# Optimization experiments

Hardware: AMD Instinct MI355X
Metric: run time of the kernel (lower is better)

Reference implementation:

```python
import jax, jax.numpy as jnp
import numpy as np

N_NODES, N_EDGES, N_CRYS = 50000, 1200000, 256
AF, NF, NR = 64, 64, 16
INV_SQRT_2 = 1.0 / 2.0 ** 0.5
EPS = 1e-5


def crystal_norm(x, idx, nseg, gamma, beta):
    # per-crystal, per-feature mean/var normalization
    cnt = jnp.maximum(jax.ops.segment_sum(jnp.ones((x.shape[0],), x.dtype), idx, nseg), 1.0)[:, None]
    mean = jax.ops.segment_sum(x, idx, nseg) / cnt
    d = x - mean[idx]
    var = jax.ops.segment_sum(d * d, idx, nseg) / cnt
    return d / jnp.sqrt(var[idx] + EPS) * gamma + beta


def setup_inputs() -> dict:
    key = jax.random.key(0)
    ks = jax.random.split(key, 16)
    s = 0.05
    return {
        'atom_fea': jax.random.normal(ks[0], (N_NODES, AF), jnp.float32),
        'edge': jax.random.normal(ks[1], (N_EDGES, NF), jnp.float32),
        'rbf': jax.random.uniform(ks[2], (N_EDGES, NR), jnp.float32),
        'nbr_fea_idx': jax.random.randint(ks[3], (N_EDGES, 2), 0, N_NODES),
        'crystal_atom_idx': jax.random.randint(ks[4], (N_NODES,), 0, N_CRYS),
        'crystal_edge_idx': jax.random.randint(ks[5], (N_EDGES,), 0, N_CRYS),
        'W_rbf': jax.random.normal(ks[6], (NR, NF), jnp.float32) * s,
        'W_full': jax.random.normal(ks[7], (2 * AF + NF, 2 * AF), jnp.float32) * s,
        'W_mask': jax.random.normal(ks[8], (AF, 1), jnp.float32) * s,
        'g1': jnp.ones((2 * AF,), jnp.float32),
        'b1': jnp.zeros((2 * AF,), jnp.float32),
        'g2': jnp.ones((AF,), jnp.float32),
        'b2': jnp.zeros((AF,), jnp.float32),
        'Wr1a': jax.random.normal(ks[9], (AF, AF // 2), jnp.float32) * s,
        'Wr1b': jax.random.normal(ks[10], (AF // 2, AF), jnp.float32) * s,
        'Wr2a': jax.random.normal(ks[11], (AF, AF // 2), jnp.float32) * s,
        'Wr2b': jax.random.normal(ks[12], (AF // 2, AF), jnp.float32) * s,
    }


def reference(atom_fea, edge, rbf, nbr_fea_idx, crystal_atom_idx, crystal_edge_idx,
              W_rbf, W_full, W_mask, g1, b1, g2, b2, Wr1a, Wr1b, Wr2a, Wr2b):
    rbf_h = rbf @ W_rbf                                   # [E, NF]
    sum_idx = nbr_fea_idx[:, 0]
    nbr_fea = edge * rbf_h                                # [E, NF]
    atom_nbr_fea = atom_fea[nbr_fea_idx].reshape(-1, 2 * AF)  # [E, 2*AF]
    total = jnp.concatenate([atom_nbr_fea, nbr_fea], axis=1)  # [E, 2*AF+NF]
    gated = total @ W_full                                # [E, 2*AF]
    gated = crystal_norm(gated, crystal_edge_idx, N_CRYS, g1, b1)
    nbr_filter, nbr_core = gated[:, :AF], gated[:, AF:]
    nbr_filter = jax.nn.sigmoid(nbr_filter @ W_mask)      # [E, 1]
    nbr_core = jax.nn.relu(nbr_core)
    msg = nbr_filter * nbr_core                           # [E, AF]
    cnt = jnp.maximum(jax.ops.segment_sum(jnp.ones((msg.shape[0],), msg.dtype), sum_idx, N_NODES), 1.0)[:, None]
    nbr_sumed = jax.ops.segment_sum(msg, sum_idx, N_NODES) / cnt  # scatter-mean
    nbr_sumed = crystal_norm(nbr_sumed, crystal_atom_idx, N_CRYS, g2, b2)
    # 2 residual blocks: out = (x + relu(relu(x W_a) W_b)) / sqrt(2)
    h = jax.nn.relu(jax.nn.relu(nbr_sumed @ Wr1a) @ Wr1b)
    nbr_sumed = (nbr_sumed + h) * INV_SQRT_2
    h = jax.nn.relu(jax.nn.relu(nbr_sumed @ Wr2a) @ Wr2b)
    nbr_sumed = (nbr_sumed + h) * INV_SQRT_2
    return INV_SQRT_2 * jax.nn.relu(atom_fea + nbr_sumed)
```

## Files before the change

### kernel.cpp

```cpp
#include <hip/hip_runtime.h>
#include <hip/hip_bf16.h>

typedef __attribute__((ext_vector_type(8))) short bfrag;
typedef __attribute__((ext_vector_type(4))) float f4;

__device__ __forceinline__ unsigned short f2bf(float f){
  unsigned b = __float_as_uint(f);
  b = (b + 0x7fffu + ((b >> 16) & 1u)) >> 16;
  return (unsigned short)b;
}
__device__ __forceinline__ unsigned pk2bf(float a, float b){
  return (unsigned)f2bf(a) | ((unsigned)f2bf(b) << 16);
}
__device__ __forceinline__ float bf2f(unsigned short u){
  return __uint_as_float(((unsigned)u) << 16);
}
__device__ __forceinline__ bfrag pack8(float4 x, float4 y){
  bfrag r;
  r[0]=(short)f2bf(x.x); r[1]=(short)f2bf(x.y); r[2]=(short)f2bf(x.z); r[3]=(short)f2bf(x.w);
  r[4]=(short)f2bf(y.x); r[5]=(short)f2bf(y.y); r[6]=(short)f2bf(y.z); r[7]=(short)f2bf(y.w);
  return r;
}

__global__ __launch_bounds__(256) void k_acvt(const float* __restrict__ atom,
                                              unsigned short* __restrict__ atomBF, int total8){
  int i = blockIdx.x*256 + threadIdx.x;
  if (i >= total8) return;
  const float4* src = (const float4*)atom + (size_t)i*2;
  float4 x = src[0], y = src[1];
  *(bfrag*)(atomBF + (size_t)i*8) = pack8(x, y);
}

__global__ __launch_bounds__(64) void k_prep(const float* __restrict__ Wf, unsigned short* __restrict__ Bpack){
  int l = threadIdx.x; int f = blockIdx.x; int ks = f >> 3; int nt = f & 7;
  int kg = l >> 4; int nn = l & 15;
#pragma unroll
  for (int j = 0; j < 8; ++j){
    int k;
    if (ks < 4) k = ks*32 + kg*8 + j;
    else        k = 128 + (ks-4)*32 + ((j>>2)<<4) + kg*4 + (j&3);
    Bpack[((size_t)f*64 + l)*8 + j] = f2bf(Wf[(size_t)k*128 + nt*16 + nn]);
  }
}

__global__ __launch_bounds__(256) void k_pre(const int* __restrict__ cidxe, int E,
                                             const int* __restrict__ cidxn, int NN,
                                             const int* __restrict__ nbr,
                                             int* __restrict__ ccnte, int* __restrict__ ccntn,
                                             int* __restrict__ ncnt){
  __shared__ int he[256], hn[256];
  int t = threadIdx.x;
  he[t] = 0; hn[t] = 0;
  __syncthreads();
  for (size_t i = (size_t)blockIdx.x*256 + t; i < (size_t)E; i += (size_t)gridDim.x*256){
    atomicAdd(&he[cidxe[i]], 1);
    atomicAdd(&ncnt[nbr[2*i]], 1);
  }
  for (size_t i = (size_t)blockIdx.x*256 + t; i < (size_t)NN; i += (size_t)gridDim.x*256)
    atomicAdd(&hn[cidxn[i]], 1);
  __syncthreads();
  if (he[t]) atomicAdd(&ccnte[t], he[t]);
  if (hn[t]) atomicAdd(&ccntn[t], hn[t]);
}

__global__ __launch_bounds__(1024) void k_scans(const int* __restrict__ ncnt, int NN,
                                                int* __restrict__ offs, int* __restrict__ cursor,
                                                const int* __restrict__ ccnte, const int* __restrict__ ccntn,
                                                int* __restrict__ ceoffs, int* __restrict__ cecur,
                                                int* __restrict__ cnoffs, int* __restrict__ cncur){
  int tid = threadIdx.x;
  if (blockIdx.x == 0){
    __shared__ int part[1024];
    int chunk = (NN + 1023) >> 10;
    int base = tid*chunk;
    int s = 0;
    for (int i = 0; i < chunk; ++i){ int p = base + i; if (p < NN) s += ncnt[p]; }
    part[tid] = s;
    __syncthreads();
    for (int d = 1; d < 1024; d <<= 1){
      int v = (tid >= d) ? part[tid - d] : 0;
      __syncthreads();
      part[tid] += v;
      __syncthreads();
    }
    int run = (tid == 0) ? 0 : part[tid-1];
    for (int i = 0; i < chunk; ++i){
      int p = base + i;
      if (p < NN){ offs[p] = run; cursor[p] = run; run += ncnt[p]; }
    }
    if (tid == 1023) offs[NN] = part[1023];
  } else {
    __shared__ int sh[256];
    const int* cnt = (blockIdx.x == 2) ? ccntn : ccnte;
    int* off = (blockIdx.x == 2) ? cnoffs : ceoffs;
    int* cur = (blockIdx.x == 2) ? cncur  : cecur;
    int v = 0;
    if (tid < 256){ v = cnt[tid]; sh[tid] = v; }
    __syncthreads();
    for (int d = 1; d < 256; d <<= 1){
      int x = (tid >= d && tid < 256) ? sh[tid - d] : 0;
      __syncthreads();
      if (tid < 256) sh[tid] += x;
      __syncthreads();
    }
    if (tid < 256){
      off[tid] = sh[tid] - v; cur[tid] = sh[tid] - v;
      if (tid == 255) off[256] = sh[255];
    }
  }
}

__global__ __launch_bounds__(256) void k_scatter2(const int* __restrict__ nbr, const int* __restrict__ cidxe,
                                                  int E, int* __restrict__ cursor, int4* __restrict__ edat,
                                                  int* __restrict__ gcur, int* __restrict__ celist){
  __shared__ int lhist[256], lbase[256], lcur[256];
  int t = threadIdx.x;
  lhist[t] = 0; lcur[t] = 0;
  __syncthreads();
  int base = blockIdx.x*1024;
  int end = min(base + 1024, E);
  for (int i = base + t; i < end; i += 256) atomicAdd(&lhist[cidxe[i]], 1);
  __syncthreads();
  if (lhist[t]) lbase[t] = atomicAdd(&gcur[t], lhist[t]);
  __syncthreads();
  for (int i = base + t; i < end; i += 256){
    int cr = cidxe[i];
    int n = nbr[2*(size_t)i];
    int j = nbr[2*(size_t)i + 1];
    int pos = atomicAdd(&cursor[n], 1);
    edat[pos] = make_int4(n, j, i, cr);
    int lp = atomicAdd(&lcur[cr], 1);
    celist[lbase[cr] + lp] = pos;
  }
}

__global__ __launch_bounds__(256) void k_cscatter(const int* __restrict__ idx, int n,
                                                  int* __restrict__ gcur, int* __restrict__ outl){
  __shared__ int lhist[256], lbase[256], lcur[256];
  int t = threadIdx.x;
  lhist[t] = 0; lcur[t] = 0;
  __syncthreads();
  int base = blockIdx.x*4096;
  int end = min(base + 4096, n);
  for (int i = base + t; i < end; i += 256) atomicAdd(&lhist[idx[i]], 1);
  __syncthreads();
  if (lhist[t]) lbase[t] = atomicAdd(&gcur[t], lhist[t]);
  __syncthreads();
  for (int i = base + t; i < end; i += 256){
    int b = idx[i];
    int p = atomicAdd(&lcur[b], 1);
    outl[lbase[b] + p] = i;
  }
}

struct TileRegs {
  bfrag a0, a1, a2, a3;
  bfrag rf;
  float4 re0, re1, re2, re3;
};

__device__ __forceinline__ TileRegs load_tile(const unsigned short* __restrict__ atomBF,
                                              const float* __restrict__ edgef,
                                              const float* __restrict__ rbff, const int4* __restrict__ edat,
                                              int r0, int e16, int g, int E){
  TileRegs R;
  int er = r0 + e16;
  if (er >= E) er = 0;
  const int4 ed = edat[er];
  const unsigned short* Ai = atomBF + (size_t)ed.x*64;
  const unsigned short* Aj = atomBF + (size_t)ed.y*64;
  R.a0 = *(const bfrag*)(Ai + g*8);
  R.a1 = *(const bfrag*)(Ai + 32 + g*8);
  R.a2 = *(const bfrag*)(Aj + g*8);
  R.a3 = *(const bfrag*)(Aj + 32 + g*8);
  float4 rr0 = make_float4(0.f,0.f,0.f,0.f);
  float4 rr1 = make_float4(0.f,0.f,0.f,0.f);
  if (g < 2){
    const float4* rp = (const float4*)(rbff + (size_t)ed.z*16 + g*8);
    rr0 = rp[0]; rr1 = rp[1];
  }
  const float4* ep = (const float4*)(edgef + (size_t)ed.z*64);
  R.re0 = ep[g]; R.re1 = ep[4+g]; R.re2 = ep[8+g]; R.re3 = ep[12+g];
  R.rf = pack8(rr0, rr1);
  return R;
}

template<int FNT0, int FNT1>
__global__ __launch_bounds__(512) void k_gemm(const unsigned short* __restrict__ atomBF,
                                              const float* __restrict__ edgef,
                                              const float* __restrict__ rbff, const int4* __restrict__ edat,
                                              const float* __restrict__ Wrbf,
                                              const unsigned short* __restrict__ Bpack,
                                              unsigned short* __restrict__ gated, int gstride, int colOff,
                                              int tBase, int tEnd, int E)
{
  __shared__ uint4 sBv[3072];
  const unsigned short* sB = (const unsigned short*)sBv;
  const int bid = (blockIdx.x & 7)*(gridDim.x >> 3) + (blockIdx.x >> 3);
  const int lane = threadIdx.x & 63;
  const int wid  = (bid*512 + threadIdx.x) >> 6;
  const int nW   = gridDim.x*8;
  const int e16  = lane & 15;
  const int g    = lane >> 4;
  const f4 zero = {0.f, 0.f, 0.f, 0.f};

  {
    const uint4* src = (const uint4*)Bpack;
    for (int i = threadIdx.x; i < 3072; i += 512) sBv[i] = src[i];
  }

  bfrag wf[4];
#pragma unroll
  for (int ct = 0; ct < 4; ++ct){
#pragma unroll
    for (int i = 0; i < 8; ++i){
      float v = (g < 2) ? Wrbf[(g*8 + i)*64 + ct*16 + e16] : 0.f;
      wf[ct][i] = (short)f2bf(v);
    }
  }
  __syncthreads();

  int t = tBase + wid;
  if (t >= tEnd) return;
  TileRegs cur = load_tile(atomBF, edgef, rbff, edat, t*16, e16, g, E);

  while (true){
    const int tn = t + nW;
    const bool more = tn < tEnd;
    TileRegs nxt;
    if (more) nxt = load_tile(atomBF, edgef, rbff, edat, tn*16, e16, g, E);
    __builtin_amdgcn_sched_barrier(0);

    int er = t*16 + e16;
    const bool rowOK = er < E;
    if (!rowOK) er = 0;

    f4 h0 = __builtin_amdgcn_mfma_f32_16x16x32_bf16(wf[0], cur.rf, zero, 0, 0, 0);
    f4 h1 = __builtin_amdgcn_mfma_f32_16x16x32_bf16(wf[1], cur.rf, zero, 0, 0, 0);
    f4 h2 = __builtin_amdgcn_mfma_f32_16x16x32_bf16(wf[2], cur.rf, zero, 0, 0, 0);
    f4 h3 = __builtin_amdgcn_mfma_f32_16x16x32_bf16(wf[3], cur.rf, zero, 0, 0, 0);

    bfrag aops[6];
    aops[0] = cur.a0; aops[1] = cur.a1; aops[2] = cur.a2; aops[3] = cur.a3;
    const float* pe0 = (const float*)&cur.re0;
    const float* pe1 = (const float*)&cur.re1;
    const float* pe2 = (const float*)&cur.re2;
    const float* pe3 = (const float*)&cur.re3;
#pragma unroll
    for (int r = 0; r < 4; ++r){
      aops[4][r]   = (short)f2bf(h0[r]*pe0[r]);
      aops[4][4+r] = (short)f2bf(h1[r]*pe1[r]);
      aops[5][r]   = (short)f2bf(h2[r]*pe2[r]);
      aops[5][4+r] = (short)f2bf(h3[r]*pe3[r]);
    }

    unsigned short* orow = gated + (size_t)er*(size_t)gstride - colOff;
#pragma unroll
    for (int f_nt = FNT0; f_nt < FNT1; ++f_nt){
      const unsigned short* bls = sB + ((size_t)(f_nt*64 + lane))*8;
      f4 acc = zero;
#pragma unroll
      for (int ks = 0; ks < 6; ++ks){
        bfrag b = *(const bfrag*)(bls + (size_t)ks*4096);
        acc = __builtin_amdgcn_mfma_f32_16x16x32_bf16(b, aops[ks], acc, 0, 0, 0);
      }
      if (rowOK){
        uint2 pk;
        pk.x = pk2bf(acc[0], acc[1]);
        pk.y = pk2bf(acc[2], acc[3]);
        *(uint2*)(orow + f_nt*16 + g*4) = pk;
      }
    }

    if (!more) break;
    cur = nxt;
    t = tn;
  }
}

__global__ __launch_bounds__(256) void k_cstats128(const unsigned short* __restrict__ gated,
                                                   const int* __restrict__ coffs, const int* __restrict__ celist,
                                                   float* __restrict__ pstat){
  int cr = blockIdx.x >> 3, s = blockIdx.x & 7;
  int t = threadIdx.x, w = t >> 6, lane = t & 63;
  int sub = lane >> 4, ch = lane & 15;
  int o0 = coffs[cr], o1 = coffs[cr+1];
  long long L = o1 - o0;
  int lo = o0 + (int)(L*s/8), hi = o0 + (int)(L*(s+1)/8);
  float S[8], Q[8];
#pragma unroll
  for (int j = 0; j < 8; ++j){ S[j] = 0.f; Q[j] = 0.f; }
  for (int p = lo + w*4; p < hi; p += 16){
    int q = p + sub;
    if (q < hi){
      int e = celist[q];
      uint4 vv = *(const uint4*)(gated + (size_t)e*128 + ch*8);
      unsigned uu0 = vv.x, uu1 = vv.y, uu2 = vv.z, uu3 = vv.w;
      float a0 = bf2f((unsigned short)(uu0 & 0xffffu)), b0 = bf2f((unsigned short)(uu0 >> 16));
      float a1 = bf2f((unsigned short)(uu1 & 0xffffu)), b1 = bf2f((unsigned short)(uu1 >> 16));
      float a2 = bf2f((unsigned short)(uu2 & 0xffffu)), b2 = bf2f((unsigned short)(uu2 >> 16));
      float a3 = bf2f((unsigned short)(uu3 & 0xffffu)), b3 = bf2f((unsigned short)(uu3 >> 16));
      S[0] += a0; Q[0] += a0*a0;  S[1] += b0; Q[1] += b0*b0;
      S[2] += a1; Q[2] += a1*a1;  S[3] += b1; Q[3] += b1*b1;
      S[4] += a2; Q[4] += a2*a2;  S[5] += b2; Q[5] += b2*b2;
      S[6] += a3; Q[6] += a3*a3;  S[7] += b3; Q[7] += b3*b3;
    }
  }
#pragma unroll
  for (int j = 0; j < 8; ++j){
    S[j] += __shfl_xor(S[j], 16, 64); S[j] += __shfl_xor(S[j], 32, 64);
    Q[j] += __shfl_xor(Q[j], 16, 64); Q[j] += __shfl_xor(Q[j], 32, 64);
  }
  __shared__ float sP[4][256];
  if (sub == 0){
#pragma unroll
    for (int j = 0; j < 8; ++j){
      sP[w][ch*16 + j]     = S[j];
      sP[w][ch*16 + 8 + j] = Q[j];
    }
  }
  __syncthreads();
  float v = sP[0][t] + sP[1][t] + sP[2][t] + sP[3][t];
  pstat[((size_t)blockIdx.x << 8) + t] = v;
}

__global__ __launch_bounds__(256) void k_cstats64(const unsigned short* __restrict__ gated,
                                                  const int* __restrict__ coffs, const int* __restrict__ celist,
                                                  float* __restrict__ pstat){
  int cr = blockIdx.x >> 3, s = blockIdx.x & 7;
  int t = threadIdx.x, w = t >> 6, lane = t & 63;
  int o0 = coffs[cr], o1 = coffs[cr+1];
  long long L = o1 - o0;
  int lo = o0 + (int)(L*s/8), hi = o0 + (int)(L*(s+1)/8);
  float S=0.f, Q=0.f;
  for (int p = lo + w*8; p < hi; p += 32){
#pragma unroll
    for (int u = 0; u < 8; ++u){
      if (p + u < hi){
        int e = celist[p+u];
        float a = bf2f(gated[(size_t)e*64 + lane]);
        S += a; Q += a*a;
      }
    }
  }
  __shared__ float sP[4][128];
  sP[w][lane*2+0]=S; sP[w][lane*2+1]=Q;
  __syncthreads();
  if (t < 128){
    float v = sP[0][t] + sP[1][t] + sP[2][t] + sP[3][t];
    pstat[((size_t)blockIdx.x << 7) + t] = v;
  }
}

__global__ __launch_bounds__(256) void k_cnstats(const float* __restrict__ nacc, const int* __restrict__ ncnt,
                                                 const int* __restrict__ coffs, const int* __restrict__ cnlist,
                                                 float* __restrict__ pstat){
  int cr = blockIdx.x >> 1, s = blockIdx.x & 1;
  int t = threadIdx.x, w = t >> 6, lane = t & 63;
  int sub = lane >> 4, c4 = lane & 15;
  int o0 = coffs[cr], o1 = coffs[cr+1];
  long long L = o1 - o0;
  int lo = o0 + (int)(L*s/2), hi = o0 + (int)(L*(s+1)/2);
  float S[4], Q[4];
#pragma unroll
  for (int j = 0; j < 4; ++j){ S[j] = 0.f; Q[j] = 0.f; }
  for (int p = lo + w*4; p < hi; p += 16){
    int q = p + sub;
    if (q < hi){
      int n = cnlist[q];
      float inv = 1.f / fmaxf((float)ncnt[n], 1.f);
      float4 v = *(const float4*)(nacc + (size_t)n*64 + c4*4);
      float a0 = v.x*inv, a1 = v.y*inv, a2 = v.z*inv, a3 = v.w*inv;
      S[0] += a0; Q[0] += a0*a0;
      S[1] += a1; Q[1] += a1*a1;
      S[2] += a2; Q[2] += a2*a2;
      S[3] += a3; Q[3] += a3*a3;
    }
  }
#pragma unroll
  for (int j = 0; j < 4; ++j){
    S[j] += __shfl_xor(S[j], 16, 64); S[j] += __shfl_xor(S[j], 32, 64);
    Q[j] += __shfl_xor(Q[j], 16, 64); Q[j] += __shfl_xor(Q[j], 32, 64);
  }
  __shared__ float sP[4][128];
  if (sub == 0){
#pragma unroll
    for (int j = 0; j < 4; ++j){
      sP[w][(c4*4 + j)*2]     = S[j];
      sP[w][(c4*4 + j)*2 + 1] = Q[j];
    }
  }
  __syncthreads();
  if (t < 128){
    float v = sP[0][t] + sP[1][t] + sP[2][t] + sP[3][t];
    pstat[((size_t)blockIdx.x << 7) + t] = v;
  }
}

__global__ __launch_bounds__(256) void k_red128f(const float* __restrict__ pstat, const int* __restrict__ ccnt,
                                                 const float* __restrict__ gamma, const float* __restrict__ beta,
                                                 const float* __restrict__ Wm,
                                                 float* __restrict__ sc, float* __restrict__ sh,
                                                 float* __restrict__ w2, float* __restrict__ fb){
  int idx = blockIdx.x*256 + threadIdx.x;
  int cr = idx >> 7, col = idx & 127;
  int vS = ((col >> 3) << 4) + (col & 7);
  float S=0.f, Q=0.f;
  for (int s2 = 0; s2 < 8; ++s2){
    const float* b = pstat + ((size_t)(cr*8 + s2) << 8);
    S += b[vS]; Q += b[vS + 8];
  }
  float cnt = fmaxf((float)ccnt[cr], 1.f);
  float mean = S/cnt;
  float var = fmaxf(Q/cnt - mean*mean, 0.f);
  float r = 1.f / sqrtf(var + 1e-5f);
  float g = r*gamma[col];
  float shv = beta[col] - mean*g;
  sc[cr*128 + col] = g;
  sh[cr*128 + col] = shv;

  __shared__ float red[256];
  float contrib = 0.f;
  if (col < 64){
    float wmv = Wm[col];
    w2[cr*64 + col] = g*wmv;
    contrib = shv*wmv;
  }
  red[threadIdx.x] = contrib;
  __syncthreads();
  int lc = threadIdx.x & 127;
  for (int d = 32; d > 0; d >>= 1){
    if (lc < d) red[threadIdx.x] += red[threadIdx.x + d];
    __syncthreads();
  }
  if (lc == 0) fb[cr] = red[threadIdx.x];
}

__global__ __launch_bounds__(256) void k_red64(const float* __restrict__ pstat, int nsplit,
                                               const int* __restrict__ ccnt,
                                               const float* __restrict__ gamma, const float* __restrict__ beta,
                                               float* __restrict__ sc, float* __restrict__ sh,
                                               int stride, int colOff){
  int idx = blockIdx.x*256 + threadIdx.x;
  int cr = idx >> 6, col = idx & 63;
  int vS = col*2;
  float S=0.f, Q=0.f;
  for (int s2 = 0; s2 < nsplit; ++s2){
    const float* b = pstat + ((size_t)(cr*nsplit + s2) << 7);
    S += b[vS]; Q += b[vS+1];
  }
  float cnt = fmaxf((float)ccnt[cr], 1.f);
  float mean = S/cnt;
  float var = fmaxf(Q/cnt - mean*mean, 0.f);
  float r = 1.f / sqrtf(var + 1e-5f);
  float g = r*gamma[col];
  sc[cr*stride + colOff + col] = g;
  sh[cr*stride + colOff + col] = beta[col] - mean*g;
}

__global__ __launch_bounds__(256) void k_fprep(const float* __restrict__ scE, const float* __restrict__ shE,
                                               const float* __restrict__ Wm, float* __restrict__ w2,
                                               float* __restrict__ fb){
  int t = threadIdx.x, w = t >> 6, lane = t & 63;
  int cr = blockIdx.x*4 + w;
  float wm = Wm[lane];
  w2[cr*64 + lane] = scE[cr*128 + lane]*wm;
  float b = shE[cr*128 + lane]*wm;
#pragma unroll
  for (int d = 1; d < 64; d <<= 1) b += __shfl_xor(b, d, 64);
  if (lane == 0) fb[cr] = b;
}

__global__ __launch_bounds__(256) void k_filter(const unsigned short* __restrict__ gated, int gst,
                                                const int4* __restrict__ edat, const float* __restrict__ w2,
                                                const float* __restrict__ fb, float* __restrict__ filt, int E){
  size_t r = (size_t)blockIdx.x*256 + threadIdx.x;
  if (r >= (size_t)E) return;
  int cr = edat[r].w;
  const uint4* row = (const uint4*)(gated + r*(size_t)gst);
  const float4* wr = (const float4*)(w2 + cr*64);
  float logit = fb[cr];
#pragma unroll
  for (int j = 0; j < 8; ++j){
    uint4 v = row[j];
    float4 wa = wr[2*j], wb = wr[2*j+1];
    logit += bf2f((unsigned short)(v.x & 0xffffu))*wa.x + bf2f((unsigned short)(v.x >> 16))*wa.y;
    logit += bf2f((unsigned short)(v.y & 0xffffu))*wa.z + bf2f((unsigned short)(v.y >> 16))*wa.w;
    logit += bf2f((unsigned short)(v.z & 0xffffu))*wb.x + bf2f((unsigned short)(v.z >> 16))*wb.y;
    logit += bf2f((unsigned short)(v.w & 0xffffu))*wb.z + bf2f((unsigned short)(v.w >> 16))*wb.w;
  }
  filt[r] = 1.f / (1.f + __expf(-logit));
}

__global__ __launch_bounds__(256) void k_msgf8(const unsigned short* __restrict__ gated,
                                               const int4* __restrict__ edat,
                                               const int* __restrict__ offs,
                                               const float* __restrict__ scE, const float* __restrict__ shE,
                                               const float* __restrict__ w2, const float* __restrict__ fb,
                                               float* __restrict__ nacc, int NN){
  int w = threadIdx.x >> 6, lane = threadIdx.x & 63;
  int n = blockIdx.x*4 + w;
  if (n >= NN) return;
  int sub = lane >> 3, c8 = lane & 7;
  float a0=0.f,a1=0.f,a2=0.f,a3=0.f,a4=0.f,a5=0.f,a6=0.f,a7=0.f;
  int p0 = offs[n], p1 = offs[n+1];

  int p = p0;
  bool any = p < p1;
  int4 ed; uint4 vf, vc;
  if (any){
    int q = p + sub; if (q >= p1) q = p;
    ed = edat[q];
    vf = *(const uint4*)(gated + (size_t)q*128 + c8*8);
    vc = *(const uint4*)(gated + (size_t)q*128 + 64 + c8*8);
  }
  while (any){
    const int pn = p + 8;
    const bool anyN = pn < p1;
    int4 edN; uint4 vfN, vcN;
    if (anyN){
      int qn = pn + sub; if (qn >= p1) qn = pn;
      edN = edat[qn];
      vfN = *(const uint4*)(gated + (size_t)qn*128 + c8*8);
      vcN = *(const uint4*)(gated + (size_t)qn*128 + 64 + c8*8);
    }
    __builtin_amdgcn_sched_barrier(0);

    const bool ok = (p + sub) < p1;
    int cr = ed.w;
    const float4* wvp = (const float4*)(w2 + cr*64 + c8*8);
    float4 wv0 = wvp[0], wv1 = wvp[1];
    float part = bf2f((unsigned short)(vf.x & 0xffffu))*wv0.x
               + bf2f((unsigned short)(vf.x >> 16))*wv0.y
               + bf2f((unsigned short)(vf.y & 0xffffu))*wv0.z
               + bf2f((unsigned short)(vf.y >> 16))*wv0.w
               + bf2f((unsigned short)(vf.z & 0xffffu))*wv1.x
               + bf2f((unsigned short)(vf.z >> 16))*wv1.y
               + bf2f((unsigned short)(vf.w & 0xffffu))*wv1.z
               + bf2f((unsigned short)(vf.w >> 16))*wv1.w;
#pragma unroll
    for (int d = 1; d < 8; d <<= 1) part += __shfl_xor(part, d, 64);
    float f = 1.f / (1.f + __expf(-(part + fb[cr])));
    const float4* scp = (const float4*)(scE + cr*128 + 64 + c8*8);
    const float4* shp = (const float4*)(shE + cr*128 + 64 + c8*8);
    float4 s0 = scp[0], s1 = scp[1];
    float4 h0 = shp[0], h1 = shp[1];
    if (ok){
      a0 += f*fmaxf(bf2f((unsigned short)(vc.x & 0xffffu))*s0.x + h0.x, 0.f);
      a1 += f*fmaxf(bf2f((unsigned short)(vc.x >> 16))*s0.y + h0.y, 0.f);
      a2 += f*fmaxf(bf2f((unsigned short)(vc.y & 0xffffu))*s0.z + h0.z, 0.f);
      a3 += f*fmaxf(bf2f((unsigned short)(vc.y >> 16))*s0.w + h0.w, 0.f);
      a4 += f*fmaxf(bf2f((unsigned short)(vc.z & 0xffffu))*s1.x + h1.x, 0.f);
      a5 += f*fmaxf(bf2f((unsigned short)(vc.z >> 16))*s1.y + h1.y, 0.f);
      a6 += f*fmaxf(bf2f((unsigned short)(vc.w & 0xffffu))*s1.z + h1.z, 0.f);
      a7 += f*fmaxf(bf2f((unsigned short)(vc.w >> 16))*s1.w + h1.w, 0.f);
    }
    if (!anyN) break;
    ed = edN; vf = vfN; vc = vcN; p = pn;
  }
#pragma unroll
  for (int d = 8; d < 64; d <<= 1){
    a0 += __shfl_xor(a0, d, 64); a1 += __shfl_xor(a1, d, 64);
    a2 += __shfl_xor(a2, d, 64); a3 += __shfl_xor(a3, d, 64);
    a4 += __shfl_xor(a4, d, 64); a5 += __shfl_xor(a5, d, 64);
    a6 += __shfl_xor(a6, d, 64); a7 += __shfl_xor(a7, d, 64);
  }
  if (lane < 8){
    float4 o0; o0.x = a0; o0.y = a1; o0.z = a2; o0.w = a3;
    float4 o1; o1.x = a4; o1.y = a5; o1.z = a6; o1.w = a7;
    float4* dst = (float4*)(nacc + (size_t)n*64 + (size_t)c8*8);
    dst[0] = o0; dst[1] = o1;
  }
}

__global__ __launch_bounds__(256) void k_msg3(const unsigned short* __restrict__ gated, int gst, int colBase,
                                              const int4* __restrict__ edat, const float* __restrict__ filt,
                                              const int* __restrict__ offs,
                                              const float* __restrict__ scE, const float* __restrict__ shE,
                                              int scOff, float* __restrict__ nacc, int NN){
  int w = threadIdx.x >> 6, lane = threadIdx.x & 63;
  int n = blockIdx.x*4 + w;
  if (n >= NN) return;
  int sub = lane >> 5, c2 = lane & 31;
  float a0 = 0.f, a1 = 0.f;
  int p0 = offs[n], p1 = offs[n+1];
  for (int p = p0; p < p1; p += 2){
    int idx = p + sub;
    bool ok = idx < p1;
    int q = ok ? idx : p;
    unsigned v = *(const unsigned*)(gated + (size_t)q*gst + colBase + c2*2);
    float f = filt[q];
    int cr = edat[q].w;
    float2 sc2 = *(const float2*)(scE + cr*128 + scOff + c2*2);
    float2 sh2 = *(const float2*)(shE + cr*128 + scOff + c2*2);
    if (ok){
      float g0 = bf2f((unsigned short)(v & 0xffffu));
      float g1 = bf2f((unsigned short)(v >> 16));
      a0 += f*fmaxf(g0*sc2.x + sh2.x, 0.f);
      a1 += f*fmaxf(g1*sc2.y + sh2.y, 0.f);
    }
  }
  a0 += __shfl_xor(a0, 32, 64);
  a1 += __shfl_xor(a1, 32, 64);
  if (lane < 32) *(float2*)(nacc + (size_t)n*64 + (size_t)c2*2) = make_float2(a0, a1);
}

__global__ __launch_bounds__(256) void k_final(const float* __restrict__ nacc, const int* __restrict__ ncnt,
                                               const int* __restrict__ cidx, const float* __restrict__ nsc,
                                               const float* __restrict__ nsh, const float* __restrict__ W1a,
                                               const float* __restrict__ W1b, const float* __restrict__ W2a,
                                               const float* __restrict__ W2b, const float* __restrict__ atom,
                                               float* __restrict__ out, int NN)
{
  __shared__ float sW[4][2048];
  __shared__ float hbuf[8192];
  int tid = threadIdx.x;
  for (int i = tid; i < 2048; i += 256){
    sW[0][i] = W1a[i]; sW[1][i] = W1b[i]; sW[2][i] = W2a[i]; sW[3][i] = W2b[i];
  }
  __syncthreads();
  int n = blockIdx.x*256 + tid;
  if (n >= NN) return;
  const float ISQ2 = 0.70710678118654752440f;
  int cr = cidx[n];
  float inv = 1.f / fmaxf((float)ncnt[n], 1.f);
  float x[64];
  const float4* src = (const float4*)(nacc + (size_t)n*64);
#pragma unroll
  for (int j = 0; j < 16; ++j){
    float4 v = src[j];
    x[4*j] = v.x*inv; x[4*j+1] = v.y*inv; x[4*j+2] = v.z*inv; x[4*j+3] = v.w*inv;
  }
#pragma unroll
  for (int c = 0; c < 64; ++c)
    x[c] = x[c]*nsc[cr*64 + c] + nsh[cr*64 + c];

  for (int blk = 0; blk < 2; ++blk){
    const float* sa = sW[blk*2];
    const float* sb = sW[blk*2 + 1];
    for (int j = 0; j < 32; ++j){
      float s = 0.f;
#pragma unroll
      for (int k = 0; k < 64; ++k) s += x[k]*sa[k*32 + j];
      hbuf[tid*32 + (j ^ (tid & 31))] = fmaxf(s, 0.f);
    }
    float x2[64];
#pragma unroll
    for (int c = 0; c < 64; ++c) x2[c] = 0.f;
    for (int j = 0; j < 32; ++j){
      float hj = hbuf[tid*32 + (j ^ (tid & 31))];
#pragma unroll
      for (int c = 0; c < 64; ++c) x2[c] += hj*sb[j*64 + c];
    }
#pragma unroll
    for (int c = 0; c < 64; ++c)
      x[c] = (x[c] + fmaxf(x2[c], 0.f))*ISQ2;
  }
  const float4* ap = (const float4*)(atom + (size_t)n*64);
  float4* op = (float4*)(out + (size_t)n*64);
#pragma unroll
  for (int j = 0; j < 16; ++j){
    float4 av = ap[j]; float4 o;
    o.x = ISQ2*fmaxf(av.x + x[4*j],   0.f);
    o.y = ISQ2*fmaxf(av.y + x[4*j+1], 0.f);
    o.z = ISQ2*fmaxf(av.z + x[4*j+2], 0.f);
    o.w = ISQ2*fmaxf(av.w + x[4*j+3], 0.f);
    op[j] = o;
  }
}

extern "C" void kernel_launch(void* const* d_in, const int* in_sizes, int n_in,
                              void* d_out, int out_size, void* d_ws, size_t ws_size,
                              hipStream_t stream)
{
  const float* atom  = (const float*)d_in[0];
  const float* edgef = (const float*)d_in[1];
  const float* rbff  = (const float*)d_in[2];
  const int*   nbr   = (const int*)d_in[3];
  const int*   cidxn = (const int*)d_in[4];
  const int*   cidxe = (const int*)d_in[5];
  const float* Wrbf  = (const float*)d_in[6];
  const float* Wful  = (const float*)d_in[7];
  const float* Wmask = (const float*)d_in[8];
  const float* g1    = (const float*)d_in[9];
  const float* b1    = (const float*)d_in[10];
  const float* g2    = (const float*)d_in[11];
  const float* b2    = (const float*)d_in[12];
  const float* W1a   = (const float*)d_in[13];
  const float* W1b   = (const float*)d_in[14];
  const float* W2a   = (const float*)d_in[15];
  const float* W2b   = (const float*)d_in[16];
  float* out = (float*)d_out;

  const int E  = in_sizes[1] / 64;
  const int NN = in_sizes[0] / 64;
  const int nT = (E + 15) / 16;

  char* p = (char*)d_ws;
  auto take = [&](size_t bytes){ void* r = (void*)p; p += (bytes + 255) & ~(size_t)255; return r; };

  const bool full = ws_size >= (size_t)360000000;
  const int gstride = full ? 128 : 64;

  unsigned short* gated = (unsigned short*)take((size_t)E*gstride*2);
  float* pstat  = (float*)take((size_t)2048*256*4);
  float* pstatN = (float*)take((size_t)512*128*4);
  float* nacc   = (float*)take((size_t)NN*64*4);
  int*   ncnt   = (int*)take((size_t)NN*4);
  int*   offs   = (int*)take((size_t)(NN+1)*4);
  int*   cursor = (int*)take((size_t)NN*4);
  int4*  edat   = (int4*)take((size_t)E*16);
  int*   celist = (int*)take((size_t)E*4);
  int*   cnlist = (int*)take((size_t)NN*4);
  int*   ceoffs = (int*)take(257*4);
  int*   cecur  = (int*)take(256*4);
  int*   cnoffs = (int*)take(257*4);
  int*   cncur  = (int*)take(256*4);
  int*   ccnte  = (int*)take(1024);
  int*   ccntn  = (int*)take(1024);
  float* scE    = (float*)take(256*128*4);
  float* shE    = (float*)take(256*128*4);
  float* nsc    = (float*)take(256*64*4);
  float* nsh    = (float*)take(256*64*4);
  float* w2     = (float*)take(256*64*4);
  float* fb     = (float*)take(256*4);
  float* filt   = (float*)take((size_t)E*4);
  unsigned short* Bpack = (unsigned short*)take(6*8*64*8*2);
  unsigned short* atomBF = (unsigned short*)take((size_t)NN*64*2);

  (void)hipMemsetAsync(ncnt,  0, (size_t)NN*4, stream);
  (void)hipMemsetAsync(ccnte, 0, 1024, stream);
  (void)hipMemsetAsync(ccntn, 0, 1024, stream);

  k_prep<<<48, 64, 0, stream>>>(Wful, Bpack);
  k_acvt<<<(NN*8 + 255)/256, 256, 0, stream>>>(atom, atomBF, NN*8);
  k_pre<<<2048, 256, 0, stream>>>(cidxe, E, cidxn, NN, nbr, ccnte, ccntn, ncnt);
  k_scans<<<3, 1024, 0, stream>>>(ncnt, NN, offs, cursor, ccnte, ccntn, ceoffs, cecur, cnoffs, cncur);
  k_scatter2<<<(E + 1023)/1024, 256, 0, stream>>>(nbr, cidxe, E, cursor, edat, cecur, celist);
  k_cscatter<<<(NN + 4095)/4096, 256, 0, stream>>>(cidxn, NN, cncur, cnlist);

  if (full){
    const int nT1 = (nT + 1)/2;
    k_gemm<0,8><<<1024, 512, 0, stream>>>(atomBF, edgef, rbff, edat, Wrbf, Bpack, gated, 128, 0, 0,   nT1, E);
    k_gemm<0,8><<<1024, 512, 0, stream>>>(atomBF, edgef, rbff, edat, Wrbf, Bpack, gated, 128, 0, nT1, nT,  E);
    k_cstats128<<<2048, 256, 0, stream>>>(gated, ceoffs, celist, pstat);
    k_red128f<<<128, 256, 0, stream>>>(pstat, ccnte, g1, b1, Wmask, scE, shE, w2, fb);
    k_msgf8<<<(NN + 3)/4, 256, 0, stream>>>(gated, edat, offs, scE, shE, w2, fb, nacc, NN);
  } else {
    k_gemm<0,4><<<1024, 512, 0, stream>>>(atomBF, edgef, rbff, edat, Wrbf, Bpack, gated, 64, 0, 0, nT, E);
    k_cstats64<<<2048, 256, 0, stream>>>(gated, ceoffs, celist, pstat);
    k_red64<<<64, 256, 0, stream>>>(pstat, 8, ccnte, g1, b1, scE, shE, 128, 0);
    k_fprep<<<64, 256, 0, stream>>>(scE, shE, Wmask, w2, fb);
    k_filter<<<(E + 255)/256, 256, 0, stream>>>(gated, 64, edat, w2, fb, filt, E);
    k_gemm<4,8><<<1024, 512, 0, stream>>>(atomBF, edgef, rbff, edat, Wrbf, Bpack, gated, 64, 64, 0, nT, E);
    k_cstats64<<<2048, 256, 0, stream>>>(gated, ceoffs, celist, pstat);
    k_red64<<<64, 256, 0, stream>>>(pstat, 8, ccnte, g1 + 64, b1 + 64, scE, shE, 128, 64);
    k_msg3<<<(NN + 3)/4, 256, 0, stream>>>(gated, 64, 0, edat, filt, offs, scE, shE, 64, nacc, NN);
  }

  k_cnstats<<<512, 256, 0, stream>>>(nacc, ncnt, cnoffs, cnlist, pstatN);
  k_red64<<<64, 256, 0, stream>>>(pstatN, 2, ccntn, g2, b2, nsc, nsh, 64, 0);
  k_final<<<(NN + 255)/256, 256, 0, stream>>>(nacc, ncnt, cidxn, nsc, nsh, W1a, W1b, W2a, W2b, atom, out, NN);
}
```

Measured before the change: 835.5 us.

## Precompute edge*rbf features in bf16 before GEMM, merge split GEMM launches

Adds a streaming kernel that computes nbr_fea = edge * (rbf @ W_rbf) in edge order and stores it as bf16. The GEMM then gathers 128 bytes per edge instead of 320 bytes of fp32 edge and rbf data, and no longer recomputes the small rbf MFMA. The two half-range GEMM launches become one. In exchange it adds an extra 150MB write and a separate kernel pass, and it raises the workspace threshold for the full path, which could silently switch to the slower split path if the workspace is too small.

Result: slower. 898.3 us (+7.5%).

```diff
diff --git a/kernel.cpp b/kernel.cpp
--- a/kernel.cpp
+++ b/kernel.cpp
@@ -40,6 +40,67 @@
     if (ks < 4) k = ks*32 + kg*8 + j;
     else        k = 128 + (ks-4)*32 + ((j>>2)<<4) + kg*4 + (j&3);
     Bpack[((size_t)f*64 + l)*8 + j] = f2bf(Wf[(size_t)k*128 + nt*16 + nn]);
+  }
+}
+
+__global__ __launch_bounds__(512) void k_fuse(const float* __restrict__ edgef,
+                                              const float* __restrict__ rbff,
+                                              const float* __restrict__ Wrbf,
+                                              unsigned short* __restrict__ nbrP,
+                                              int nT, int E){
+  const int lane = threadIdx.x & 63;
+  const int wid  = (blockIdx.x*512 + threadIdx.x) >> 6;
+  const int nW   = gridDim.x*8;
+  const int e16  = lane & 15;
+  const int g    = lane >> 4;
+  const f4 zero = {0.f, 0.f, 0.f, 0.f};
+
+  bfrag wf[4];
+#pragma unroll
+  for (int ct = 0; ct < 4; ++ct){
+#pragma unroll
+    for (int i = 0; i < 8; ++i){
+      float v = (g < 2) ? Wrbf[(g*8 + i)*64 + ct*16 + e16] : 0.f;
+      wf[ct][i] = (short)f2bf(v);
+    }
+  }
+
+  for (int t = wid; t < nT; t += nW){
+    int e = t*16 + e16;
+    const bool ok = e < E;
+    int ec = ok ? e : 0;
+    float4 rr0 = make_float4(0.f,0.f,0.f,0.f);
+    float4 rr1 = make_float4(0.f,0.f,0.f,0.f);
+    if (g < 2){
+      const float4* rp = (const float4*)(rbff + (size_t)ec*16 + g*8);
+      rr0 = rp[0]; rr1 = rp[1];
+    }
+    const float4* ep = (const float4*)(edgef + (size_t)ec*64);
+    float4 re0 = ep[g], re1 = ep[4+g], re2 = ep[8+g], re3 = ep[12+g];
+
+    bfrag rf = pack8(rr0, rr1);
+    f4 h0 = __builtin_amdgcn_mfma_f32_16x16x32_bf16(wf[0], rf, zero, 0, 0, 0);
+    f4 h1 = __builtin_amdgcn_mfma_f32_16x16x32_bf16(wf[1], rf, zero, 0, 0, 0);
+    f4 h2 = __builtin_amdgcn_mfma_f32_16x16x32_bf16(wf[2], rf, zero, 0, 0, 0);
+    f4 h3 = __builtin_amdgcn_mfma_f32_16x16x32_bf16(wf[3], rf, zero, 0, 0, 0);
+
+    bfrag A4, A5;
+    const float* pe0 = (const float*)&re0;
+    const float* pe1 = (const float*)&re1;
+    const float* pe2 = (const float*)&re2;
+    const float* pe3 = (const float*)&re3;
+#pragma unroll
+    for (int r = 0; r < 4; ++r){
+      A4[r]   = (short)f2bf(h0[r]*pe0[r]);
+      A4[4+r] = (short)f2bf(h1[r]*pe1[r]);
+      A5[r]   = (short)f2bf(h2[r]*pe2[r]);
+      A5[4+r] = (short)f2bf(h3[r]*pe3[r]);
+    }
+    if (ok){
+      unsigned short* np = nbrP + (size_t)e*64;
+      *(bfrag*)(np + g*8)      = A4;
+      *(bfrag*)(np + 32 + g*8) = A5;
+    }
   }
 }
 
@@ -155,13 +216,12 @@
 
 struct TileRegs {
   bfrag a0, a1, a2, a3;
-  bfrag rf;
-  float4 re0, re1, re2, re3;
+  bfrag n4, n5;
 };
 
 __device__ __forceinline__ TileRegs load_tile(const unsigned short* __restrict__ atomBF,
-                                              const float* __restrict__ edgef,
-                                              const float* __restrict__ rbff, const int4* __restrict__ edat,
+                                              const unsigned short* __restrict__ nbrP,
+                                              const int4* __restrict__ edat,
                                               int r0, int e16, int g, int E){
   TileRegs R;
   int er = r0 + e16;
@@ -173,26 +233,19 @@
   R.a1 = *(const bfrag*)(Ai + 32 + g*8);
   R.a2 = *(const bfrag*)(Aj + g*8);
   R.a3 = *(const bfrag*)(Aj + 32 + g*8);
-  float4 rr0 = make_float4(0.f,0.f,0.f,0.f);
-  float4 rr1 = make_float4(0.f,0.f,0.f,0.f);
-  if (g < 2){
-    const float4* rp = (const float4*)(rbff + (size_t)ed.z*16 + g*8);
-    rr0 = rp[0]; rr1 = rp[1];
-  }
-  const float4* ep = (const float4*)(edgef + (size_t)ed.z*64);
-  R.re0 = ep[g]; R.re1 = ep[4+g]; R.re2 = ep[8+g]; R.re3 = ep[12+g];
-  R.rf = pack8(rr0, rr1);
+  const unsigned short* np = nbrP + (size_t)ed.z*64;
+  R.n4 = *(const bfrag*)(np + g*8);
+  R.n5 = *(const bfrag*)(np + 32 + g*8);
   return R;
 }
 
 template<int FNT0, int FNT1>
 __global__ __launch_bounds__(512) void k_gemm(const unsigned short* __restrict__ atomBF,
-                                              const float* __restrict__ edgef,
-                                              const float* __restrict__ rbff, const int4* __restrict__ edat,
-                                              const float* __restrict__ Wrbf,
+                                              const unsigned short* __restrict__ nbrP,
+                                              const int4* __restrict__ edat,
                                               const unsigned short* __restrict__ Bpack,
                                               unsigned short* __restrict__ gated, int gstride, int colOff,
-                                              int tBase, int tEnd, int E)
+                                              int nT, int E)
 {
   __shared__ uint4 sBv[3072];
   const unsigned short* sB = (const unsigned short*)sBv;
@@ -208,51 +261,26 @@
     const uint4* src = (const uint4*)Bpack;
     for (int i = threadIdx.x; i < 3072; i += 512) sBv[i] = src[i];
   }
-
-  bfrag wf[4];
-#pragma unroll
-  for (int ct = 0; ct < 4; ++ct){
-#pragma unroll
-    for (int i = 0; i < 8; ++i){
-      float v = (g < 2) ? Wrbf[(g*8 + i)*64 + ct*16 + e16] : 0.f;
-      wf[ct][i] = (short)f2bf(v);
-    }
-  }
-  __syncthreads();
-
-  int t = tBase + wid;
-  if (t >= tEnd) return;
-  TileRegs cur = load_tile(atomBF, edgef, rbff, edat, t*16, e16, g, E);
+  __syncthreads();
+
+  int t = wid;
+  if (t >= nT) return;
+  TileRegs cur = load_tile(atomBF, nbrP, edat, t*16, e16, g, E);
 
   while (true){
     const int tn = t + nW;
-    const bool more = tn < tEnd;
+    const bool more = tn < nT;
     TileRegs nxt;
-    if (more) nxt = load_tile(atomBF, edgef, rbff, edat, tn*16, e16, g, E);
+    if (more) nxt = load_tile(atomBF, nbrP, edat, tn*16, e16, g, E);
     __builtin_amdgcn_sched_barrier(0);
 
     int er = t*16 + e16;
     const bool rowOK = er < E;
     if (!rowOK) er = 0;
 
-    f4 h0 = __builtin_amdgcn_mfma_f32_16x16x32_bf16(wf[0], cur.rf, zero, 0, 0, 0);
-    f4 h1 = __builtin_amdgcn_mfma_f32_16x16x32_bf16(wf[1], cur.rf, zero, 0, 0, 0);
-    f4 h2 = __builtin_amdgcn_mfma_f32_16x16x32_bf16(wf[2], cur.rf, zero, 0, 0, 0);
-    f4 h3 = __builtin_amdgcn_mfma_f32_16x16x32_bf16(wf[3], cur.rf, zero, 0, 0, 0);
-
     bfrag aops[6];
     aops[0] = cur.a0; aops[1] = cur.a1; aops[2] = cur.a2; aops[3] = cur.a3;
-    const float* pe0 = (const float*)&cur.re0;
-    const float* pe1 = (const float*)&cur.re1;
-    const float* pe2 = (const float*)&cur.re2;
-    const float* pe3 = (const float*)&cur.re3;
-#pragma unroll
-    for (int r = 0; r < 4; ++r){
-      aops[4][r]   = (short)f2bf(h0[r]*pe0[r]);
-      aops[4][4+r] = (short)f2bf(h1[r]*pe1[r]);
-      aops[5][r]   = (short)f2bf(h2[r]*pe2[r]);
-      aops[5][4+r] = (short)f2bf(h3[r]*pe3[r]);
-    }
+    aops[4] = cur.n4; aops[5] = cur.n5;
 
     unsigned short* orow = gated + (size_t)er*(size_t)gstride - colOff;
 #pragma unroll
@@ -699,7 +727,7 @@
   char* p = (char*)d_ws;
   auto take = [&](size_t bytes){ void* r = (void*)p; p += (bytes + 255) & ~(size_t)255; return r; };
 
-  const bool full = ws_size >= (size_t)360000000;
+  const bool full = ws_size >= (size_t)560000000;
   const int gstride = full ? 128 : 64;
 
   unsigned short* gated = (unsigned short*)take((size_t)E*gstride*2);
@@ -727,6 +755,7 @@
   float* filt   = (float*)take((size_t)E*4);
   unsigned short* Bpack = (unsigned short*)take(6*8*64*8*2);
   unsigned short* atomBF = (unsigned short*)take((size_t)NN*64*2);
+  unsigned short* nbrP   = (unsigned short*)take((size_t)E*64*2);
 
   (void)hipMemsetAsync(ncnt,  0, (size_t)NN*4, stream);
   (void)hipMemsetAsync(ccnte, 0, 1024, stream);
@@ -734,25 +763,24 @@
 
   k_prep<<<48, 64, 0, stream>>>(Wful, Bpack);
   k_acvt<<<(NN*8 + 255)/256, 256, 0, stream>>>(atom, atomBF, NN*8);
+  k_fuse<<<1024, 512, 0, stream>>>(edgef, rbff, Wrbf, nbrP, nT, E);
   k_pre<<<2048, 256, 0, stream>>>(cidxe, E, cidxn, NN, nbr, ccnte, ccntn, ncnt);
   k_scans<<<3, 1024, 0, stream>>>(ncnt, NN, offs, cursor, ccnte, ccntn, ceoffs, cecur, cnoffs, cncur);
   k_scatter2<<<(E + 1023)/1024, 256, 0, stream>>>(nbr, cidxe, E, cursor, edat, cecur, celist);
   k_cscatter<<<(NN + 4095)/4096, 256, 0, stream>>>(cidxn, NN, cncur, cnlist);
 
   if (full){
-    const int nT1 = (nT + 1)/2;
-    k_gemm<0,8><<<1024, 512, 0, stream>>>(atomBF, edgef, rbff, edat, Wrbf, Bpack, gated, 128, 0, 0,   nT1, E);
-    k_gemm<0,8><<<1024, 512, 0, stream>>>(atomBF, edgef, rbff, edat, Wrbf, Bpack, gated, 128, 0, nT1, nT,  E);
+    k_gemm<0,8><<<1024, 512, 0, stream>>>(atomBF, nbrP, edat, Bpack, gated, 128, 0, nT, E);
     k_cstats128<<<2048, 256, 0, stream>>>(gated, ceoffs, celist, pstat);
     k_red128f<<<128, 256, 0, stream>>>(pstat, ccnte, g1, b1, Wmask, scE, shE, w2, fb);
     k_msgf8<<<(NN + 3)/4, 256, 0, stream>>>(gated, edat, offs, scE, shE, w2, fb, nacc, NN);
   } else {
-    k_gemm<0,4><<<1024, 512, 0, stream>>>(atomBF, edgef, rbff, edat, Wrbf, Bpack, gated, 64, 0, 0, nT, E);
+    k_gemm<0,4><<<1024, 512, 0, stream>>>(atomBF, nbrP, edat, Bpack, gated, 64, 0, nT, E);
     k_cstats64<<<2048, 256, 0, stream>>>(gated, ceoffs, celist, pstat);
     k_red64<<<64, 256, 0, stream>>>(pstat, 8, ccnte, g1, b1, scE, shE, 128, 0);
     k_fprep<<<64, 256, 0, stream>>>(scE, shE, Wmask, w2, fb);
     k_filter<<<(E + 255)/256, 256, 0, stream>>>(gated, 64, edat, w2, fb, filt, E);
-    k_gemm<4,8><<<1024, 512, 0, stream>>>(atomBF, edgef, rbff, edat, Wrbf, Bpack, gated, 64, 64, 0, nT, E);
+    k_gemm<4,8><<<1024, 512, 0, stream>>>(atomBF, nbrP, edat, Bpack, gated, 64, 64, nT, E);
     k_cstats64<<<2048, 256, 0, stream>>>(gated, ceoffs, celist, pstat);
     k_red64<<<64, 256, 0, stream>>>(pstat, 8, ccnte, g1 + 64, b1 + 64, scE, shE, 128, 64);
     k_msg3<<<(NN + 3)/4, 256, 0, stream>>>(gated, 64, 0, edat, filt, offs, scE, shE, 64, nacc, NN);
```
